# Performance work log

Hardware: AMD Instinct MI355X
Metric: run time of the kernel (lower is better)

Reference implementation:

```python
import jax, jax.numpy as jnp
import numpy as np

N, E, D, H, G = 50000, 640000, 128, 128, 64
EPS = 1e-5


def gcn_conv(x, row, col, W, b, n):
    # PyG GCNConv: linear transform, symmetric deg^-1/2 normalization (self-loops
    # already appended to row/col), scatter-add aggregation, then bias.
    h = x @ W  # [N, H]
    ones = jnp.ones(row.shape[0], dtype=h.dtype)
    deg = jax.ops.segment_sum(ones, col, num_segments=n)
    dinv = jnp.where(deg > 0, jax.lax.rsqrt(deg), 0.0)
    norm = dinv[row] * dinv[col]                       # [E+N]
    msg = h[row] * norm[:, None]                       # gather + scale
    out = jax.ops.segment_sum(msg, col, num_segments=n)  # scatter-add
    return out + b


def graph_layernorm(x, w, b):
    # PyG LayerNorm(mode='graph') with batch=None: normalize over the whole tensor.
    mu = x.mean()
    xc = x - mu
    std = jnp.sqrt((xc * xc).mean())
    return xc / (std + EPS) * w + b


def setup_inputs() -> dict:
    key = jax.random.key(0)
    ks = jax.random.split(key, 12)
    x = jax.random.normal(ks[0], (N, D), dtype=jnp.float32)
    edge_index = jax.random.randint(ks[1], (2, E), 0, N, dtype=jnp.int64)
    batch = jnp.sort(jax.random.randint(ks[2], (N,), 0, G, dtype=jnp.int64))
    s1 = 1.0 / np.sqrt(D)
    s2 = 1.0 / np.sqrt(H)
    return {
        "x": x,
        "edge_index": edge_index,
        "batch": batch,
        "W1": jax.random.normal(ks[3], (D, H), dtype=jnp.float32) * s1,
        "b1": jnp.zeros((H,), dtype=jnp.float32),
        "ln1_w": jnp.ones((H,), dtype=jnp.float32),
        "ln1_b": jnp.zeros((H,), dtype=jnp.float32),
        "W2": jax.random.normal(ks[4], (H, H), dtype=jnp.float32) * s2,
        "b2": jnp.zeros((H,), dtype=jnp.float32),
        "ln2_w": jnp.ones((H,), dtype=jnp.float32),
        "ln2_b": jnp.zeros((H,), dtype=jnp.float32),
        "fc_w": jax.random.normal(ks[5], (H, 1), dtype=jnp.float32) * s2,
        "fc_b": jnp.zeros((1,), dtype=jnp.float32),
    }


def reference(x, edge_index, batch, W1, b1, ln1_w, ln1_b, W2, b2, ln2_w, ln2_b, fc_w, fc_b):
    n = x.shape[0]
    loops = jnp.arange(n, dtype=edge_index.dtype)
    row = jnp.concatenate([edge_index[0], loops])  # add self-loops
    col = jnp.concatenate([edge_index[1], loops])

    h = gcn_conv(x, row, col, W1, b1, n)
    h = jax.nn.relu(graph_layernorm(h, ln1_w, ln1_b))
    h = gcn_conv(h, row, col, W2, b2, n)
    h = jax.nn.relu(graph_layernorm(h, ln2_w, ln2_b))

    # global_mean_pool over batch segment ids
    sums = jax.ops.segment_sum(h, batch, num_segments=G)          # [G, H]
    cnt = jax.ops.segment_sum(jnp.ones((n,), h.dtype), batch, num_segments=G)
    pooled = sums / jnp.maximum(cnt, 1.0)[:, None]

    logits = pooled @ fc_w + fc_b                                  # [G, 1]
    return jax.nn.sigmoid(logits).squeeze(-1)                      # [G]
```

## Files before the change

### kernel.cpp

```cpp
#include <hip/hip_runtime.h>
#include <math.h>

#define H 128
#define PC 16

typedef _Float16 half8v __attribute__((ext_vector_type(8)));
typedef float floatx4 __attribute__((ext_vector_type(4)));

__device__ __forceinline__ int lower_bound_i(const int* a, int n, int key) {
  int lo = 0, hi = n;
  while (lo < hi) { int mid = (lo + hi) >> 1; if (a[mid] < key) lo = mid + 1; else hi = mid; }
  return lo;
}

__global__ void k_init(const float* __restrict__ W1, const float* __restrict__ W2,
                       _Float16* __restrict__ PW1, _Float16* __restrict__ PW2,
                       int* cntE, float* slots, int* esrc,
                       float* glog, int* gdone, int* total,
                       int cap, int n, int g) {
  int b = blockIdx.x;
  int tid = threadIdx.x;
  if (b < 128) {
    int t = b * 256 + tid;
    const float* W = (t < 16384) ? W1 : W2;
    _Float16* PW = (t < 16384) ? PW1 : PW2;
    int u = t & 16383;
    int j = u & 7;
    int nn = (u >> 3) & 15;
    int quad = (u >> 7) & 3;
    int ks = (u >> 9) & 3;
    int ct = (u >> 11) & 7;
    PW[u] = (_Float16)W[(ks * 32 + quad * 8 + j) * H + ct * 16 + nn];
  } else {
    int i = (b - 128) * 256 + tid;
    int stride = 128 * 256;
    for (int j = i; j < n; j += stride) cntE[j] = 0;
    for (int j = i; j < 256; j += stride) slots[j] = 0.f;
    for (int j = i; j < cap; j += stride) esrc[j] = n;
    for (int j = i; j < g; j += stride) { glog[j] = 0.f; gdone[j] = 0; }
    if (i == 0) *total = 0;
  }
}

__global__ void k_count(const int* __restrict__ col, int* __restrict__ cntE,
                        int* __restrict__ perm, int E) {
  int e = blockIdx.x * blockDim.x + threadIdx.x;
  if (e < E) perm[e] = atomicAdd(&cntE[col[e]], 1);
}

__global__ __launch_bounds__(256) void k_alloc(const int* __restrict__ cnt,
                                               int* __restrict__ offs,
                                               float* __restrict__ dinv,
                                               int* __restrict__ total, int n) {
  __shared__ int ws[4];
  __shared__ int base_sh;
  int tid = threadIdx.x;
  int i = blockIdx.x * 256 + tid;
  int c = (i < n) ? cnt[i] : 0;
  int v = (i < n) ? ((c + 15) & ~15) : 0;
  int lane = tid & 63;
  int wid = tid >> 6;
  int incl = v;
#pragma unroll
  for (int o = 1; o < 64; o <<= 1) {
    int t = __shfl_up(incl, o, 64);
    if (lane >= o) incl += t;
  }
  if (lane == 63) ws[wid] = incl;
  __syncthreads();
  if (tid == 0) {
    int s = 0;
#pragma unroll
    for (int w = 0; w < 4; w++) { int t = ws[w]; ws[w] = s; s += t; }
    base_sh = atomicAdd(total, s);
  }
  __syncthreads();
  if (i < n) {
    offs[i] = base_sh + ws[wid] + (incl - v);
    dinv[i] = rsqrtf((float)(c + 1));
  }
}

__device__ __forceinline__ void gemm_tile_f32(const float* __restrict__ Xf,
                                              const _Float16* __restrict__ PW,
                                              const float* __restrict__ dinv,
                                              _Float16* __restrict__ O,
                                              int wave, int laneid, int n) {
  int m = laneid & 15;
  int quad = laneid >> 4;
  int r0 = wave * 16;
  int row = r0 + m;
  if (row >= n) row = n - 1;
  floatx4 acc[8] = {};
  const half8v* PB8 = (const half8v*)PW;
#pragma unroll
  for (int ks = 0; ks < 4; ks++) {
    int kb = ks * 32 + quad * 8;
    const float* xr = Xf + (size_t)row * H + kb;
    float4 u0 = *(const float4*)xr;
    float4 u1 = *(const float4*)(xr + 4);
    half8v a;
    a[0] = (_Float16)u0.x; a[1] = (_Float16)u0.y; a[2] = (_Float16)u0.z; a[3] = (_Float16)u0.w;
    a[4] = (_Float16)u1.x; a[5] = (_Float16)u1.y; a[6] = (_Float16)u1.z; a[7] = (_Float16)u1.w;
#pragma unroll
    for (int ct = 0; ct < 8; ct++) {
      half8v b = PB8[((ct * 4 + ks) * 4 + quad) * 16 + m];
      acc[ct] = __builtin_amdgcn_mfma_f32_16x16x32_f16(a, b, acc[ct], 0, 0, 0);
    }
  }
  float dv[4];
#pragma unroll
  for (int reg = 0; reg < 4; reg++) {
    int ro = r0 + quad * 4 + reg;
    dv[reg] = (ro < n) ? dinv[ro] : 0.f;
  }
#pragma unroll
  for (int ct = 0; ct < 8; ct++) {
#pragma unroll
    for (int reg = 0; reg < 4; reg++) {
      int ro = r0 + quad * 4 + reg;
      if (ro < n) O[(size_t)ro * H + ct * 16 + m] = (_Float16)(acc[ct][reg] * dv[reg]);
    }
  }
}

__global__ __launch_bounds__(256) void k_sg1(const int* __restrict__ row, const int* __restrict__ col,
                                             const int* __restrict__ offs, const int* __restrict__ perm,
                                             int* __restrict__ esrc, int E,
                                             const float* __restrict__ Xf,
                                             const _Float16* __restrict__ PW,
                                             const float* __restrict__ dinv,
                                             _Float16* __restrict__ O, int n, int GB) {
  int b = blockIdx.x;
  if (b < GB) {
    if (b == 0 && threadIdx.x < 16) {
      half8v z = {};
      *(half8v*)&O[(size_t)n * H + threadIdx.x * 8] = z;
    }
    int wave = b * 4 + (threadIdx.x >> 6);
    int tiles = (n + 15) >> 4;
    if (wave >= tiles) return;
    gemm_tile_f32(Xf, PW, dinv, O, wave, threadIdx.x & 63, n);
  } else {
    int e = (b - GB) * 256 + threadIdx.x;
    if (e < E) {
      int c = col[e];
      esrc[offs[c] + perm[e]] = row[e];
    }
  }
}

__global__ __launch_bounds__(256) void k_agg(const _Float16* __restrict__ Gs,
                                             _Float16* __restrict__ Out,
                                             const int* __restrict__ esrc, const int* __restrict__ offs,
                                             const int* __restrict__ cntE, const float* __restrict__ dinv,
                                             const float* __restrict__ bias, float* __restrict__ slot,
                                             int n) {
  int sub = threadIdx.x >> 4;
  int lane = threadIdx.x & 15;
  int i = blockIdx.x * 16 + sub;
  float sv = 0.f, sq = 0.f;
  if (i < n) {
    float di = dinv[i];
    half8v gself = *(const half8v*)&Gs[(size_t)i * H + 8 * lane];
    float acc[8];
#pragma unroll
    for (int e = 0; e < 8; e++) acc[e] = (float)gself[e];
    int beg = offs[i];
    int c16 = (cntE[i] + 15) & ~15;
    int sid = (c16 > 0) ? esrc[beg + lane] : 0;
    for (int base = 0; base < c16; base += 16) {
      int cur = sid;
      if (base + 16 < c16) sid = esrc[beg + base + 16 + lane];
      int sg[16]; half8v hg[16];
#pragma unroll
      for (int u = 0; u < 16; u++) sg[u] = __shfl(cur, u, 16);
#pragma unroll
      for (int u = 0; u < 16; u++) hg[u] = *(const half8v*)&Gs[(size_t)sg[u] * H + 8 * lane];
#pragma unroll
      for (int e = 0; e < 8; e++) {
        float t0 = 0.f, t1 = 0.f;
#pragma unroll
        for (int u = 0; u < 8; u++) { t0 += (float)hg[u][e]; t1 += (float)hg[8 + u][e]; }
        acc[e] += t0 + t1;
      }
    }
    const float* bb = bias + 8 * lane;
    half8v vo;
#pragma unroll
    for (int e = 0; e < 8; e++) {
      float v = di * acc[e] + bb[e];
      vo[e] = (_Float16)v;
      sv += v;
      sq += v * v;
    }
    *(half8v*)&Out[(size_t)i * H + 8 * lane] = vo;
  }
#pragma unroll
  for (int o = 32; o > 0; o >>= 1) {
    sv += __shfl_xor(sv, o, 64);
    sq += __shfl_xor(sq, o, 64);
  }
  __shared__ float rsm[4], rqm[4];
  int wave = threadIdx.x >> 6;
  if ((threadIdx.x & 63) == 0) { rsm[wave] = sv; rqm[wave] = sq; }
  __syncthreads();
  if (threadIdx.x == 0) {
    float ts = rsm[0] + rsm[1] + rsm[2] + rsm[3];
    float tq = rqm[0] + rqm[1] + rqm[2] + rqm[3];
    int sl = blockIdx.x & 63;
    atomicAdd(&slot[sl], ts);
    atomicAdd(&slot[64 + sl], tq);
  }
}

__global__ __launch_bounds__(256) void k_gemm2(const _Float16* __restrict__ Xh,
                                               const _Float16* __restrict__ PW,
                                               const float* __restrict__ lnw,
                                               const float* __restrict__ lnb,
                                               const float* __restrict__ slot, float invM,
                                               const float* __restrict__ dinv,
                                               _Float16* __restrict__ O, int n) {
  if (blockIdx.x == 0 && threadIdx.x < 16) {
    half8v z = {};
    *(half8v*)&O[(size_t)n * H + threadIdx.x * 8] = z;
  }
  int wave = blockIdx.x * 4 + (threadIdx.x >> 6);
  int tiles = (n + 15) >> 4;
  if (wave >= tiles) return;
  int lane = threadIdx.x & 63;
  int m = lane & 15;
  int quad = lane >> 4;
  int r0 = wave * 16;
  int row = r0 + m;
  if (row >= n) row = n - 1;

  float s = slot[lane], q = slot[64 + lane];
#pragma unroll
  for (int o = 32; o > 0; o >>= 1) { s += __shfl_xor(s, o, 64); q += __shfl_xor(q, o, 64); }
  float mu = s * invM;
  float var = fmaxf(q * invM - mu * mu, 0.f);
  float rs = 1.f / (sqrtf(var) + 1e-5f);

  floatx4 acc[8] = {};
  const half8v* PB8 = (const half8v*)PW;
#pragma unroll
  for (int ks = 0; ks < 4; ks++) {
    int kb = ks * 32 + quad * 8;
    half8v hv = *(const half8v*)(Xh + (size_t)row * H + kb);
    float4 w0 = *(const float4*)(lnw + kb);
    float4 w1 = *(const float4*)(lnw + kb + 4);
    float4 c0 = *(const float4*)(lnb + kb);
    float4 c1 = *(const float4*)(lnb + kb + 4);
    half8v a;
    a[0] = (_Float16)fmaxf(((float)hv[0] - mu) * rs * w0.x + c0.x, 0.f);
    a[1] = (_Float16)fmaxf(((float)hv[1] - mu) * rs * w0.y + c0.y, 0.f);
    a[2] = (_Float16)fmaxf(((float)hv[2] - mu) * rs * w0.z + c0.z, 0.f);
    a[3] = (_Float16)fmaxf(((float)hv[3] - mu) * rs * w0.w + c0.w, 0.f);
    a[4] = (_Float16)fmaxf(((float)hv[4] - mu) * rs * w1.x + c1.x, 0.f);
    a[5] = (_Float16)fmaxf(((float)hv[5] - mu) * rs * w1.y + c1.y, 0.f);
    a[6] = (_Float16)fmaxf(((float)hv[6] - mu) * rs * w1.z + c1.z, 0.f);
    a[7] = (_Float16)fmaxf(((float)hv[7] - mu) * rs * w1.w + c1.w, 0.f);
#pragma unroll
    for (int ct = 0; ct < 8; ct++) {
      half8v b = PB8[((ct * 4 + ks) * 4 + quad) * 16 + m];
      acc[ct] = __builtin_amdgcn_mfma_f32_16x16x32_f16(a, b, acc[ct], 0, 0, 0);
    }
  }
  float dv[4];
#pragma unroll
  for (int reg = 0; reg < 4; reg++) {
    int ro = r0 + quad * 4 + reg;
    dv[reg] = (ro < n) ? dinv[ro] : 0.f;
  }
#pragma unroll
  for (int ct = 0; ct < 8; ct++) {
#pragma unroll
    for (int reg = 0; reg < 4; reg++) {
      int ro = r0 + quad * 4 + reg;
      if (ro < n) O[(size_t)ro * H + ct * 16 + m] = (_Float16)(acc[ct][reg] * dv[reg]);
    }
  }
}

__global__ __launch_bounds__(128) void k_poolfc(const _Float16* __restrict__ Hs,
                                                const int* __restrict__ batch,
                                                const float* __restrict__ lnw, const float* __restrict__ lnb,
                                                const float* __restrict__ slot, float invM,
                                                const float* __restrict__ fcw, const float* __restrict__ fcb,
                                                float* __restrict__ glog, int* __restrict__ gdone,
                                                float* __restrict__ out, int n) {
  int g = blockIdx.x / PC, q = blockIdx.x % PC;
  int t = threadIdx.x;
  int l = t & 63;
  float s = slot[l], qq = slot[64 + l];
#pragma unroll
  for (int o = 32; o > 0; o >>= 1) { s += __shfl_xor(s, o, 64); qq += __shfl_xor(qq, o, 64); }
  float mu = s * invM;
  float var = fmaxf(qq * invM - mu * mu, 0.f);
  float rs = 1.f / (sqrtf(var) + 1e-5f);

  int start = lower_bound_i(batch, n, g);
  int end = lower_bound_i(batch, n, g + 1);
  int tot = end - start;
  int per = (tot + PC - 1) / PC;
  int s0 = start + q * per;
  int e0 = s0 + per; if (e0 > end) e0 = end;
  float w = lnw[t], bb = lnb[t];
  float acc = 0.f;
  for (int i = s0; i < e0; i++) {
    float v = (float)Hs[(size_t)i * H + t];
    v = (v - mu) * rs * w + bb;
    acc += fmaxf(v, 0.f);
  }
  float cnt = fmaxf((float)tot, 1.f);
  float v = acc * fcw[t] / cnt;
  int wave = t >> 6;
#pragma unroll
  for (int o = 32; o > 0; o >>= 1) v += __shfl_xor(v, o, 64);
  __shared__ float r2[2];
  if (l == 0) r2[wave] = v;
  __syncthreads();
  if (t == 0) {
    float part = r2[0] + r2[1];
    atomicAdd(&glog[g], part);
    __threadfence();
    int old = atomicAdd(&gdone[g], 1);
    if (old == PC - 1) {
      float totv = atomicAdd(&glog[g], 0.0f);
      out[g] = 1.f / (1.f + expf(-(totv + fcb[0])));
    }
  }
}

extern "C" void kernel_launch(void* const* d_in, const int* in_sizes, int n_in,
                              void* d_out, int out_size, void* d_ws, size_t ws_size,
                              hipStream_t stream) {
  const float* x    = (const float*)d_in[0];
  const int*   ei   = (const int*)d_in[1];
  const int*   batch= (const int*)d_in[2];
  const float* W1   = (const float*)d_in[3];
  const float* b1   = (const float*)d_in[4];
  const float* ln1w = (const float*)d_in[5];
  const float* ln1b = (const float*)d_in[6];
  const float* W2   = (const float*)d_in[7];
  const float* b2   = (const float*)d_in[8];
  const float* ln2w = (const float*)d_in[9];
  const float* ln2b = (const float*)d_in[10];
  const float* fcw  = (const float*)d_in[11];
  const float* fcb  = (const float*)d_in[12];
  float* out = (float*)d_out;

  int N = in_sizes[2];
  int E = in_sizes[1] / 2;
  int G = out_size;
  int CAP = E + 15 * N;

  char* p = (char*)d_ws;
  int*   cntE   = (int*)p;   p += (size_t)N * 4;
  int*   offs   = (int*)p;   p += (size_t)N * 4;
  float* dinv   = (float*)p; p += (size_t)N * 4;
  int*   perm   = (int*)p;   p += (size_t)E * 4;
  int*   esrc   = (int*)p;   p += (size_t)CAP * 4;
  _Float16* bufA = (_Float16*)p; p += (size_t)(N + 1) * H * 2;
  _Float16* bufB = (_Float16*)p; p += (size_t)(N + 1) * H * 2;
  _Float16* PW1  = (_Float16*)p; p += 16384 * 2;
  _Float16* PW2  = (_Float16*)p; p += 16384 * 2;
  float* slots  = (float*)p; p += 256 * 4;
  float* glog   = (float*)p; p += (size_t)G * 4;
  int*   gdone  = (int*)p;   p += (size_t)G * 4;
  int*   total  = (int*)p;   p += 4;

  const int* row = ei;
  const int* col = ei + E;

  int EB = (E + 255) / 256;
  int NB = (N + 255) / 256;
  int tiles = (N + 15) / 16;
  int GB = (tiles + 3) / 4;
  float invM = 1.f / ((float)N * (float)H);

  k_init<<<256, 256, 0, stream>>>(W1, W2, PW1, PW2, cntE, slots, esrc, glog, gdone, total, CAP, N, G);
  k_count<<<EB, 256, 0, stream>>>(col, cntE, perm, E);
  k_alloc<<<NB, 256, 0, stream>>>(cntE, offs, dinv, total, N);
  k_sg1<<<GB + EB, 256, 0, stream>>>(row, col, offs, perm, esrc, E, x, PW1, dinv, bufA, N, GB);
  k_agg<<<(N + 15) / 16, 256, 0, stream>>>(bufA, bufB, esrc, offs, cntE, dinv, b1, slots, N);
  k_gemm2<<<GB, 256, 0, stream>>>(bufB, PW2, ln1w, ln1b, slots, invM, dinv, bufA, N);
  k_agg<<<(N + 15) / 16, 256, 0, stream>>>(bufA, bufB, esrc, offs, cntE, dinv, b2, slots + 128, N);
  k_poolfc<<<G * PC, 128, 0, stream>>>(bufB, batch, ln2w, ln2b, slots + 128, invM, fcw, fcb,
                                       glog, gdone, out, N);
}
```

Before: 267.3 us.

## Fuse all stages into one persistent kernel with hierarchical grid barriers

```diff
diff --git a/kernel.cpp b/kernel.cpp
--- a/kernel.cpp
+++ b/kernel.cpp
@@ -3,9 +3,31 @@
 
 #define H 128
 #define PC 16
+#define GRID_BLOCKS 512
+
+#define MAGIC0 0x13572468
+#define MAGIC1 0x2468ACE1
 
 typedef _Float16 half8v __attribute__((ext_vector_type(8)));
 typedef float floatx4 __attribute__((ext_vector_type(4)));
+
+struct KParams {
+  const float* x;
+  const int* row;
+  const int* col;
+  const int* batch;
+  const float* W1; const float* b1; const float* ln1w; const float* ln1b;
+  const float* W2; const float* b2; const float* ln2w; const float* ln2b;
+  const float* fcw; const float* fcb;
+  float* out;
+  int* cntE; int* offs; float* dinv; int* perm; int* esrc;
+  _Float16* bufA; _Float16* bufB;
+  _Float16* PW1; _Float16* PW2;
+  float* slots; float* glog; int* total;
+  int* bar_leaf; int* bar_root; int* bar_gen; int* bar_flag;
+  int N; int E; int G; int CAP;
+  float invM;
+};
 
 __device__ __forceinline__ int lower_bound_i(const int* a, int n, int key) {
   int lo = 0, hi = n;
@@ -13,72 +35,28 @@
   return lo;
 }
 
-__global__ void k_init(const float* __restrict__ W1, const float* __restrict__ W2,
-                       _Float16* __restrict__ PW1, _Float16* __restrict__ PW2,
-                       int* cntE, float* slots, int* esrc,
-                       float* glog, int* gdone, int* total,
-                       int cap, int n, int g) {
-  int b = blockIdx.x;
-  int tid = threadIdx.x;
-  if (b < 128) {
-    int t = b * 256 + tid;
-    const float* W = (t < 16384) ? W1 : W2;
-    _Float16* PW = (t < 16384) ? PW1 : PW2;
-    int u = t & 16383;
-    int j = u & 7;
-    int nn = (u >> 3) & 15;
-    int quad = (u >> 7) & 3;
-    int ks = (u >> 9) & 3;
-    int ct = (u >> 11) & 7;
-    PW[u] = (_Float16)W[(ks * 32 + quad * 8 + j) * H + ct * 16 + nn];
-  } else {
-    int i = (b - 128) * 256 + tid;
-    int stride = 128 * 256;
-    for (int j = i; j < n; j += stride) cntE[j] = 0;
-    for (int j = i; j < 256; j += stride) slots[j] = 0.f;
-    for (int j = i; j < cap; j += stride) esrc[j] = n;
-    for (int j = i; j < g; j += stride) { glog[j] = 0.f; gdone[j] = 0; }
-    if (i == 0) *total = 0;
-  }
-}
-
-__global__ void k_count(const int* __restrict__ col, int* __restrict__ cntE,
-                        int* __restrict__ perm, int E) {
-  int e = blockIdx.x * blockDim.x + threadIdx.x;
-  if (e < E) perm[e] = atomicAdd(&cntE[col[e]], 1);
-}
-
-__global__ __launch_bounds__(256) void k_alloc(const int* __restrict__ cnt,
-                                               int* __restrict__ offs,
-                                               float* __restrict__ dinv,
-                                               int* __restrict__ total, int n) {
-  __shared__ int ws[4];
-  __shared__ int base_sh;
-  int tid = threadIdx.x;
-  int i = blockIdx.x * 256 + tid;
-  int c = (i < n) ? cnt[i] : 0;
-  int v = (i < n) ? ((c + 15) & ~15) : 0;
-  int lane = tid & 63;
-  int wid = tid >> 6;
-  int incl = v;
-#pragma unroll
-  for (int o = 1; o < 64; o <<= 1) {
-    int t = __shfl_up(incl, o, 64);
-    if (lane >= o) incl += t;
-  }
-  if (lane == 63) ws[wid] = incl;
+__device__ __forceinline__ void gridbar(int* leaf, int* root, int* gen) {
   __syncthreads();
-  if (tid == 0) {
-    int s = 0;
-#pragma unroll
-    for (int w = 0; w < 4; w++) { int t = ws[w]; ws[w] = s; s += t; }
-    base_sh = atomicAdd(total, s);
+  if (threadIdx.x == 0) {
+    __threadfence();
+    int g = __hip_atomic_load(gen, __ATOMIC_RELAXED, __HIP_MEMORY_SCOPE_AGENT);
+    int nb = gridDim.x;
+    int li = blockIdx.x & 63;
+    int lc = nb >> 6;
+    if (atomicAdd(&leaf[li], 1) == lc - 1) {
+      atomicExch(&leaf[li], 0);
+      __threadfence();
+      if (atomicAdd(root, 1) == 63) {
+        atomicExch(root, 0);
+        __threadfence();
+        atomicAdd(gen, 1);
+      }
+    }
+    while (__hip_atomic_load(gen, __ATOMIC_RELAXED, __HIP_MEMORY_SCOPE_AGENT) == g)
+      __builtin_amdgcn_s_sleep(2);
+    __threadfence();
   }
   __syncthreads();
-  if (i < n) {
-    offs[i] = base_sh + ws[wid] + (incl - v);
-    dinv[i] = rsqrtf((float)(c + 1));
-  }
 }
 
 __device__ __forceinline__ void gemm_tile_f32(const float* __restrict__ Xf,
@@ -124,124 +102,19 @@
   }
 }
 
-__global__ __launch_bounds__(256) void k_sg1(const int* __restrict__ row, const int* __restrict__ col,
-                                             const int* __restrict__ offs, const int* __restrict__ perm,
-                                             int* __restrict__ esrc, int E,
-                                             const float* __restrict__ Xf,
-                                             const _Float16* __restrict__ PW,
-                                             const float* __restrict__ dinv,
-                                             _Float16* __restrict__ O, int n, int GB) {
-  int b = blockIdx.x;
-  if (b < GB) {
-    if (b == 0 && threadIdx.x < 16) {
-      half8v z = {};
-      *(half8v*)&O[(size_t)n * H + threadIdx.x * 8] = z;
-    }
-    int wave = b * 4 + (threadIdx.x >> 6);
-    int tiles = (n + 15) >> 4;
-    if (wave >= tiles) return;
-    gemm_tile_f32(Xf, PW, dinv, O, wave, threadIdx.x & 63, n);
-  } else {
-    int e = (b - GB) * 256 + threadIdx.x;
-    if (e < E) {
-      int c = col[e];
-      esrc[offs[c] + perm[e]] = row[e];
-    }
-  }
-}
-
-__global__ __launch_bounds__(256) void k_agg(const _Float16* __restrict__ Gs,
-                                             _Float16* __restrict__ Out,
-                                             const int* __restrict__ esrc, const int* __restrict__ offs,
-                                             const int* __restrict__ cntE, const float* __restrict__ dinv,
-                                             const float* __restrict__ bias, float* __restrict__ slot,
-                                             int n) {
-  int sub = threadIdx.x >> 4;
-  int lane = threadIdx.x & 15;
-  int i = blockIdx.x * 16 + sub;
-  float sv = 0.f, sq = 0.f;
-  if (i < n) {
-    float di = dinv[i];
-    half8v gself = *(const half8v*)&Gs[(size_t)i * H + 8 * lane];
-    float acc[8];
-#pragma unroll
-    for (int e = 0; e < 8; e++) acc[e] = (float)gself[e];
-    int beg = offs[i];
-    int c16 = (cntE[i] + 15) & ~15;
-    int sid = (c16 > 0) ? esrc[beg + lane] : 0;
-    for (int base = 0; base < c16; base += 16) {
-      int cur = sid;
-      if (base + 16 < c16) sid = esrc[beg + base + 16 + lane];
-      int sg[16]; half8v hg[16];
-#pragma unroll
-      for (int u = 0; u < 16; u++) sg[u] = __shfl(cur, u, 16);
-#pragma unroll
-      for (int u = 0; u < 16; u++) hg[u] = *(const half8v*)&Gs[(size_t)sg[u] * H + 8 * lane];
-#pragma unroll
-      for (int e = 0; e < 8; e++) {
-        float t0 = 0.f, t1 = 0.f;
-#pragma unroll
-        for (int u = 0; u < 8; u++) { t0 += (float)hg[u][e]; t1 += (float)hg[8 + u][e]; }
-        acc[e] += t0 + t1;
-      }
-    }
-    const float* bb = bias + 8 * lane;
-    half8v vo;
-#pragma unroll
-    for (int e = 0; e < 8; e++) {
-      float v = di * acc[e] + bb[e];
-      vo[e] = (_Float16)v;
-      sv += v;
-      sq += v * v;
-    }
-    *(half8v*)&Out[(size_t)i * H + 8 * lane] = vo;
-  }
-#pragma unroll
-  for (int o = 32; o > 0; o >>= 1) {
-    sv += __shfl_xor(sv, o, 64);
-    sq += __shfl_xor(sq, o, 64);
-  }
-  __shared__ float rsm[4], rqm[4];
-  int wave = threadIdx.x >> 6;
-  if ((threadIdx.x & 63) == 0) { rsm[wave] = sv; rqm[wave] = sq; }
-  __syncthreads();
-  if (threadIdx.x == 0) {
-    float ts = rsm[0] + rsm[1] + rsm[2] + rsm[3];
-    float tq = rqm[0] + rqm[1] + rqm[2] + rqm[3];
-    int sl = blockIdx.x & 63;
-    atomicAdd(&slot[sl], ts);
-    atomicAdd(&slot[64 + sl], tq);
-  }
-}
-
-__global__ __launch_bounds__(256) void k_gemm2(const _Float16* __restrict__ Xh,
-                                               const _Float16* __restrict__ PW,
-                                               const float* __restrict__ lnw,
-                                               const float* __restrict__ lnb,
-                                               const float* __restrict__ slot, float invM,
-                                               const float* __restrict__ dinv,
-                                               _Float16* __restrict__ O, int n) {
-  if (blockIdx.x == 0 && threadIdx.x < 16) {
-    half8v z = {};
-    *(half8v*)&O[(size_t)n * H + threadIdx.x * 8] = z;
-  }
-  int wave = blockIdx.x * 4 + (threadIdx.x >> 6);
-  int tiles = (n + 15) >> 4;
-  if (wave >= tiles) return;
-  int lane = threadIdx.x & 63;
-  int m = lane & 15;
-  int quad = lane >> 4;
+__device__ __forceinline__ void gemm2_tile(const _Float16* __restrict__ Xh,
+                                           const _Float16* __restrict__ PW,
+                                           const float* __restrict__ lnw,
+                                           const float* __restrict__ lnb,
+                                           float mu, float rs,
+                                           const float* __restrict__ dinv,
+                                           _Float16* __restrict__ O,
+                                           int wave, int laneid, int n) {
+  int m = laneid & 15;
+  int quad = laneid >> 4;
   int r0 = wave * 16;
   int row = r0 + m;
   if (row >= n) row = n - 1;
-
-  float s = slot[lane], q = slot[64 + lane];
-#pragma unroll
-  for (int o = 32; o > 0; o >>= 1) { s += __shfl_xor(s, o, 64); q += __shfl_xor(q, o, 64); }
-  float mu = s * invM;
-  float var = fmaxf(q * invM - mu * mu, 0.f);
-  float rs = 1.f / (sqrtf(var) + 1e-5f);
-
   floatx4 acc[8] = {};
   const half8v* PB8 = (const half8v*)PW;
 #pragma unroll
@@ -283,54 +156,254 @@
   }
 }
 
-__global__ __launch_bounds__(128) void k_poolfc(const _Float16* __restrict__ Hs,
-                                                const int* __restrict__ batch,
-                                                const float* __restrict__ lnw, const float* __restrict__ lnb,
-                                                const float* __restrict__ slot, float invM,
-                                                const float* __restrict__ fcw, const float* __restrict__ fcb,
-                                                float* __restrict__ glog, int* __restrict__ gdone,
-                                                float* __restrict__ out, int n) {
-  int g = blockIdx.x / PC, q = blockIdx.x % PC;
-  int t = threadIdx.x;
-  int l = t & 63;
-  float s = slot[l], qq = slot[64 + l];
-#pragma unroll
-  for (int o = 32; o > 0; o >>= 1) { s += __shfl_xor(s, o, 64); qq += __shfl_xor(qq, o, 64); }
-  float mu = s * invM;
-  float var = fmaxf(qq * invM - mu * mu, 0.f);
-  float rs = 1.f / (sqrtf(var) + 1e-5f);
-
-  int start = lower_bound_i(batch, n, g);
-  int end = lower_bound_i(batch, n, g + 1);
-  int tot = end - start;
-  int per = (tot + PC - 1) / PC;
-  int s0 = start + q * per;
-  int e0 = s0 + per; if (e0 > end) e0 = end;
-  float w = lnw[t], bb = lnb[t];
-  float acc = 0.f;
-  for (int i = s0; i < e0; i++) {
-    float v = (float)Hs[(size_t)i * H + t];
-    v = (v - mu) * rs * w + bb;
-    acc += fmaxf(v, 0.f);
-  }
-  float cnt = fmaxf((float)tot, 1.f);
-  float v = acc * fcw[t] / cnt;
-  int wave = t >> 6;
-#pragma unroll
-  for (int o = 32; o > 0; o >>= 1) v += __shfl_xor(v, o, 64);
-  __shared__ float r2[2];
-  if (l == 0) r2[wave] = v;
-  __syncthreads();
-  if (t == 0) {
-    float part = r2[0] + r2[1];
-    atomicAdd(&glog[g], part);
-    __threadfence();
-    int old = atomicAdd(&gdone[g], 1);
-    if (old == PC - 1) {
-      float totv = atomicAdd(&glog[g], 0.0f);
-      out[g] = 1.f / (1.f + expf(-(totv + fcb[0])));
-    }
-  }
+__device__ __forceinline__ void agg_group(const _Float16* __restrict__ Gs,
+                                          _Float16* __restrict__ Out,
+                                          const int* __restrict__ esrc,
+                                          const int* __restrict__ offs,
+                                          const int* __restrict__ cntE,
+                                          const float* __restrict__ dinv,
+                                          const float* __restrict__ bias,
+                                          int i, int lane, int n,
+                                          float& sv, float& sq) {
+  if (i >= n) return;
+  float di = dinv[i];
+  half8v gself = *(const half8v*)&Gs[(size_t)i * H + 8 * lane];
+  float acc[8];
+#pragma unroll
+  for (int e = 0; e < 8; e++) acc[e] = (float)gself[e];
+  int beg = offs[i];
+  int c16 = (cntE[i] + 15) & ~15;
+  int sid = (c16 > 0) ? esrc[beg + lane] : 0;
+  for (int base = 0; base < c16; base += 16) {
+    int cur = sid;
+    if (base + 16 < c16) sid = esrc[beg + base + 16 + lane];
+    int sg[16]; half8v hg[16];
+#pragma unroll
+    for (int u = 0; u < 16; u++) sg[u] = __shfl(cur, u, 16);
+#pragma unroll
+    for (int u = 0; u < 16; u++) hg[u] = *(const half8v*)&Gs[(size_t)sg[u] * H + 8 * lane];
+#pragma unroll
+    for (int e = 0; e < 8; e++) {
+      float t0 = 0.f, t1 = 0.f;
+#pragma unroll
+      for (int u = 0; u < 8; u++) { t0 += (float)hg[u][e]; t1 += (float)hg[8 + u][e]; }
+      acc[e] += t0 + t1;
+    }
+  }
+  const float* bb = bias + 8 * lane;
+  half8v vo;
+#pragma unroll
+  for (int e = 0; e < 8; e++) {
+    float v = di * acc[e] + bb[e];
+    vo[e] = (_Float16)v;
+    sv += v;
+    sq += v * v;
+  }
+  *(half8v*)&Out[(size_t)i * H + 8 * lane] = vo;
+}
+
+__global__ __launch_bounds__(256, 2) void k_fused(KParams P) {
+  const int tid = threadIdx.x;
+  const int bid = blockIdx.x;
+  const int nb = gridDim.x;
+  const int gtid = bid * 256 + tid;
+  const int gstride = nb * 256;
+  const int n = P.N, E = P.E, G_ = P.G;
+  int* BL = P.bar_leaf; int* BR = P.bar_root; int* BG = P.bar_gen;
+
+  {
+    __shared__ int s_need;
+    if (bid == 0) {
+      if (tid == 0) {
+        int f0 = __hip_atomic_load(&P.bar_flag[0], __ATOMIC_RELAXED, __HIP_MEMORY_SCOPE_AGENT);
+        int f1 = __hip_atomic_load(&P.bar_flag[1], __ATOMIC_RELAXED, __HIP_MEMORY_SCOPE_AGENT);
+        s_need = !(f0 == MAGIC0 && f1 == MAGIC1);
+      }
+      __syncthreads();
+      if (s_need) {
+        if (tid < 64) atomicExch(&BL[tid], 0);
+        if (tid == 0) { atomicExch(BR, 0); atomicExch(BG, 0); }
+      }
+      __syncthreads();
+      if (tid == 0 && s_need) {
+        __threadfence();
+        atomicExch(&P.bar_flag[0], MAGIC0);
+        atomicExch(&P.bar_flag[1], MAGIC1);
+      }
+    } else {
+      if (tid == 0) {
+        while (!(__hip_atomic_load(&P.bar_flag[0], __ATOMIC_RELAXED, __HIP_MEMORY_SCOPE_AGENT) == MAGIC0 &&
+                 __hip_atomic_load(&P.bar_flag[1], __ATOMIC_RELAXED, __HIP_MEMORY_SCOPE_AGENT) == MAGIC1))
+          __builtin_amdgcn_s_sleep(2);
+        __threadfence();
+      }
+      __syncthreads();
+    }
+  }
+
+  for (int t = gtid; t < 32768; t += gstride) {
+    const float* W = (t < 16384) ? P.W1 : P.W2;
+    _Float16* PW = (t < 16384) ? P.PW1 : P.PW2;
+    int u = t & 16383;
+    int j = u & 7;
+    int nn = (u >> 3) & 15;
+    int quad = (u >> 7) & 3;
+    int ks = (u >> 9) & 3;
+    int ct = (u >> 11) & 7;
+    PW[u] = (_Float16)W[(ks * 32 + quad * 8 + j) * H + ct * 16 + nn];
+  }
+  for (int j = gtid; j < n; j += gstride) P.cntE[j] = 0;
+  for (int j = gtid; j < 256; j += gstride) P.slots[j] = 0.f;
+  for (int j = gtid; j < P.CAP; j += gstride) P.esrc[j] = n;
+  for (int j = gtid; j < G_; j += gstride) P.glog[j] = 0.f;
+  if (gtid == 0) *P.total = 0;
+  {
+    half8v z = {};
+    if (gtid < 16) *(half8v*)&P.bufA[(size_t)n * H + gtid * 8] = z;
+    else if (gtid < 32) *(half8v*)&P.bufB[(size_t)n * H + (gtid - 16) * 8] = z;
+  }
+  gridbar(BL, BR, BG);
+
+  for (int e = gtid; e < E; e += gstride) P.perm[e] = atomicAdd(&P.cntE[P.col[e]], 1);
+  gridbar(BL, BR, BG);
+
+  {
+    __shared__ int ws[4];
+    __shared__ int base_sh;
+    int nchunks = (n + 255) >> 8;
+    int lane = tid & 63, wid = tid >> 6;
+    for (int ch = bid; ch < nchunks; ch += nb) {
+      int i = ch * 256 + tid;
+      int c = (i < n) ? P.cntE[i] : 0;
+      int v = (i < n) ? ((c + 15) & ~15) : 0;
+      int incl = v;
+#pragma unroll
+      for (int o = 1; o < 64; o <<= 1) {
+        int t2 = __shfl_up(incl, o, 64);
+        if (lane >= o) incl += t2;
+      }
+      if (lane == 63) ws[wid] = incl;
+      __syncthreads();
+      if (tid == 0) {
+        int s = 0;
+#pragma unroll
+        for (int w = 0; w < 4; w++) { int t2 = ws[w]; ws[w] = s; s += t2; }
+        base_sh = atomicAdd(P.total, s);
+      }
+      __syncthreads();
+      if (i < n) {
+        P.offs[i] = base_sh + ws[wid] + (incl - v);
+        P.dinv[i] = rsqrtf((float)(c + 1));
+      }
+      __syncthreads();
+    }
+  }
+  gridbar(BL, BR, BG);
+
+  for (int e = gtid; e < E; e += gstride) {
+    int c = P.col[e];
+    P.esrc[P.offs[c] + P.perm[e]] = P.row[e];
+  }
+  {
+    int tiles = (n + 15) >> 4;
+    int gw = bid * 4 + (tid >> 6), nw = nb * 4, lane = tid & 63;
+    for (int w = gw; w < tiles; w += nw) gemm_tile_f32(P.x, P.PW1, P.dinv, P.bufA, w, lane, n);
+  }
+  gridbar(BL, BR, BG);
+
+  {
+    int ngroups = (n + 15) >> 4;
+    int sub = tid >> 4, lane = tid & 15;
+    float sv = 0.f, sq = 0.f;
+    for (int gr = bid; gr < ngroups; gr += nb)
+      agg_group(P.bufA, P.bufB, P.esrc, P.offs, P.cntE, P.dinv, P.b1, gr * 16 + sub, lane, n, sv, sq);
+#pragma unroll
+    for (int o = 32; o > 0; o >>= 1) { sv += __shfl_xor(sv, o, 64); sq += __shfl_xor(sq, o, 64); }
+    __shared__ float rsm1[4], rqm1[4];
+    int wid = tid >> 6;
+    if ((tid & 63) == 0) { rsm1[wid] = sv; rqm1[wid] = sq; }
+    __syncthreads();
+    if (tid == 0) {
+      atomicAdd(&P.slots[bid & 63], rsm1[0] + rsm1[1] + rsm1[2] + rsm1[3]);
+      atomicAdd(&P.slots[64 + (bid & 63)], rqm1[0] + rqm1[1] + rqm1[2] + rqm1[3]);
+    }
+  }
+  gridbar(BL, BR, BG);
+
+  {
+    int lane64 = tid & 63;
+    float s = P.slots[lane64], q = P.slots[64 + lane64];
+#pragma unroll
+    for (int o = 32; o > 0; o >>= 1) { s += __shfl_xor(s, o, 64); q += __shfl_xor(q, o, 64); }
+    float mu = s * P.invM;
+    float var = fmaxf(q * P.invM - mu * mu, 0.f);
+    float rs = 1.f / (sqrtf(var) + 1e-5f);
+    int tiles = (n + 15) >> 4;
+    int gw = bid * 4 + (tid >> 6), nw = nb * 4;
+    for (int w = gw; w < tiles; w += nw)
+      gemm2_tile(P.bufB, P.PW2, P.ln1w, P.ln1b, mu, rs, P.dinv, P.bufA, w, lane64, n);
+  }
+  gridbar(BL, BR, BG);
+
+  {
+    int ngroups = (n + 15) >> 4;
+    int sub = tid >> 4, lane = tid & 15;
+    float sv = 0.f, sq = 0.f;
+    for (int gr = bid; gr < ngroups; gr += nb)
+      agg_group(P.bufA, P.bufB, P.esrc, P.offs, P.cntE, P.dinv, P.b2, gr * 16 + sub, lane, n, sv, sq);
+#pragma unroll
+    for (int o = 32; o > 0; o >>= 1) { sv += __shfl_xor(sv, o, 64); sq += __shfl_xor(sq, o, 64); }
+    __shared__ float rsm2[4], rqm2[4];
+    int wid = tid >> 6;
+    if ((tid & 63) == 0) { rsm2[wid] = sv; rqm2[wid] = sq; }
+    __syncthreads();
+    if (tid == 0) {
+      atomicAdd(&P.slots[128 + (bid & 63)], rsm2[0] + rsm2[1] + rsm2[2] + rsm2[3]);
+      atomicAdd(&P.slots[192 + (bid & 63)], rqm2[0] + rqm2[1] + rqm2[2] + rqm2[3]);
+    }
+  }
+  gridbar(BL, BR, BG);
+
+  {
+    int lane64 = tid & 63;
+    float s = P.slots[128 + lane64], q = P.slots[192 + lane64];
+#pragma unroll
+    for (int o = 32; o > 0; o >>= 1) { s += __shfl_xor(s, o, 64); q += __shfl_xor(q, o, 64); }
+    float mu = s * P.invM;
+    float var = fmaxf(q * P.invM - mu * mu, 0.f);
+    float rs = 1.f / (sqrtf(var) + 1e-5f);
+
+    int half = tid >> 7;
+    int t = tid & 127;
+    int nch = G_ * PC;
+    for (int base = bid * 2; base < nch; base += nb * 2) {
+      int c = base + half;
+      if (c < nch) {
+        int g = c / PC, qch = c % PC;
+        int start = lower_bound_i(P.batch, n, g);
+        int end = lower_bound_i(P.batch, n, g + 1);
+        int tot = end - start;
+        int per = (tot + PC - 1) / PC;
+        int s0 = start + qch * per;
+        int e0 = s0 + per; if (e0 > end) e0 = end;
+        float w = P.ln2w[t], bb = P.ln2b[t];
+        float acc = 0.f;
+        for (int i = s0; i < e0; i++) {
+          float v = (float)P.bufB[(size_t)i * H + t];
+          v = (v - mu) * rs * w + bb;
+          acc += fmaxf(v, 0.f);
+        }
+        float cnt = fmaxf((float)tot, 1.f);
+        float v = acc * P.fcw[t] / cnt;
+#pragma unroll
+        for (int o = 32; o > 0; o >>= 1) v += __shfl_xor(v, o, 64);
+        if ((t & 63) == 0) atomicAdd(&P.glog[g], v);
+      }
+    }
+  }
+  gridbar(BL, BR, BG);
+
+  if (gtid < G_) P.out[gtid] = 1.f / (1.f + expf(-(P.glog[gtid] + P.fcb[0])));
 }
 
 extern "C" void kernel_launch(void* const* d_in, const int* in_sizes, int n_in,
@@ -368,25 +441,24 @@
   _Float16* PW2  = (_Float16*)p; p += 16384 * 2;
   float* slots  = (float*)p; p += 256 * 4;
   float* glog   = (float*)p; p += (size_t)G * 4;
-  int*   gdone  = (int*)p;   p += (size_t)G * 4;
   int*   total  = (int*)p;   p += 4;
-
-  const int* row = ei;
-  const int* col = ei + E;
-
-  int EB = (E + 255) / 256;
-  int NB = (N + 255) / 256;
-  int tiles = (N + 15) / 16;
-  int GB = (tiles + 3) / 4;
-  float invM = 1.f / ((float)N * (float)H);
-
-  k_init<<<256, 256, 0, stream>>>(W1, W2, PW1, PW2, cntE, slots, esrc, glog, gdone, total, CAP, N, G);
-  k_count<<<EB, 256, 0, stream>>>(col, cntE, perm, E);
-  k_alloc<<<NB, 256, 0, stream>>>(cntE, offs, dinv, total, N);
-  k_sg1<<<GB + EB, 256, 0, stream>>>(row, col, offs, perm, esrc, E, x, PW1, dinv, bufA, N, GB);
-  k_agg<<<(N + 15) / 16, 256, 0, stream>>>(bufA, bufB, esrc, offs, cntE, dinv, b1, slots, N);
-  k_gemm2<<<GB, 256, 0, stream>>>(bufB, PW2, ln1w, ln1b, slots, invM, dinv, bufA, N);
-  k_agg<<<(N + 15) / 16, 256, 0, stream>>>(bufA, bufB, esrc, offs, cntE, dinv, b2, slots + 128, N);
-  k_poolfc<<<G * PC, 128, 0, stream>>>(bufB, batch, ln2w, ln2b, slots + 128, invM, fcw, fcb,
-                                       glog, gdone, out, N);
-}
+  int*   bleaf  = (int*)p;   p += 64 * 4;
+  int*   broot  = (int*)p;   p += 4;
+  int*   bgen   = (int*)p;   p += 4;
+  int*   bflag  = (int*)p;   p += 2 * 4;
+
+  KParams kp;
+  kp.x = x; kp.row = ei; kp.col = ei + E; kp.batch = batch;
+  kp.W1 = W1; kp.b1 = b1; kp.ln1w = ln1w; kp.ln1b = ln1b;
+  kp.W2 = W2; kp.b2 = b2; kp.ln2w = ln2w; kp.ln2b = ln2b;
+  kp.fcw = fcw; kp.fcb = fcb;
+  kp.out = out;
+  kp.cntE = cntE; kp.offs = offs; kp.dinv = dinv; kp.perm = perm; kp.esrc = esrc;
+  kp.bufA = bufA; kp.bufB = bufB; kp.PW1 = PW1; kp.PW2 = PW2;
+  kp.slots = slots; kp.glog = glog; kp.total = total;
+  kp.bar_leaf = bleaf; kp.bar_root = broot; kp.bar_gen = bgen; kp.bar_flag = bflag;
+  kp.N = N; kp.E = E; kp.G = G; kp.CAP = CAP;
+  kp.invM = 1.f / ((float)N * (float)H);
+
+  k_fused<<<dim3(GRID_BLOCKS), dim3(256), 0, stream>>>(kp);
+}
```

After: 490.6 us. 83.6% more time.
